# Kernel tuning notes

Measured on AMD Instinct MI355X. Metric: run time of the kernel, lower is better.

The kernel has to match this reference:

```python
import jax, jax.numpy as jnp
import numpy as np

B, CI, HI, WI = 64, 3, 96, 96
G = 8
HG, WG = 16, 16
HIDLIN = 512
SIGMA_BOOST = 2.0
EPS = 1e-7
HID = (HI // 4 // 2) * (WI // 4 // 2) * 128  # 12*12*128 = 18432


def _conv(x, w, b):
    # NCHW conv, 3x3, padding 1 (matches nn.Conv2d(kernel_size=3, padding=1))
    y = jax.lax.conv_general_dilated(x, w, (1, 1), ((1, 1), (1, 1)),
                                     dimension_numbers=('NCHW', 'OIHW', 'NCHW'))
    return y + b[None, :, None, None]


def _maxpool(x, k):
    return jax.lax.reduce_window(x, -jnp.inf, jax.lax.max,
                                 (1, 1, k, k), (1, 1, k, k), 'VALID')


def setup_inputs() -> dict:
    key = jax.random.key(0)
    ks = jax.random.split(key, 22)

    def w(k, shape, fan_in):
        return jax.random.normal(k, shape, jnp.float32) * np.float32(1.0 / np.sqrt(fan_in))

    return {
        'image': jax.random.normal(ks[0], (B, CI, HI, WI), jnp.float32),
        'noise': jax.random.normal(ks[1], (B * G, 2), jnp.float32),
        # conv block 1
        'w1a': w(ks[2], (32, CI, 3, 3), CI * 9), 'b1a': jnp.zeros((32,), jnp.float32),
        'w1b': w(ks[3], (32, 32, 3, 3), 32 * 9), 'b1b': jnp.zeros((32,), jnp.float32),
        # conv block 2
        'w2a': w(ks[4], (64, 32, 3, 3), 32 * 9), 'b2a': jnp.zeros((64,), jnp.float32),
        'w2b': w(ks[5], (64, 64, 3, 3), 64 * 9), 'b2b': jnp.zeros((64,), jnp.float32),
        # conv block 3
        'w3a': w(ks[6], (128, 64, 3, 3), 64 * 9), 'b3a': jnp.zeros((128,), jnp.float32),
        'w3b': w(ks[7], (128, 128, 3, 3), 128 * 9), 'b3b': jnp.zeros((128,), jnp.float32),
        # linear head (weights stored (in, out))
        'wl1': w(ks[8], (HID, HIDLIN), HID), 'bl1': jnp.zeros((HIDLIN,), jnp.float32),
        'wl2': w(ks[9], (HIDLIN, HIDLIN), HIDLIN), 'bl2': jnp.zeros((HIDLIN,), jnp.float32),
        'wl3': w(ks[10], (HIDLIN, G * 3), HIDLIN), 'bl3': jnp.zeros((G * 3,), jnp.float32),
    }


def reference(image, noise, w1a, b1a, w1b, b1b, w2a, b2a, w2b, b2b,
              w3a, b3a, w3b, b3b, wl1, bl1, wl2, bl2, wl3, bl3):
    # --- preprocess CNN ---
    x = jax.nn.relu(_conv(image, w1a, b1a))
    x = jax.nn.relu(_conv(x, w1b, b1b))
    x = _maxpool(x, 4)
    x = jax.nn.relu(_conv(x, w2a, b2a))
    x = jax.nn.relu(_conv(x, w2b, b2b))
    x = _maxpool(x, 2)
    x = jax.nn.relu(_conv(x, w3a, b3a))
    x = jax.nn.relu(_conv(x, w3b, b3b))
    x = x.reshape(B, -1)                      # Flatten (C,H,W order, like torch .view)
    x = jax.nn.relu(x @ wl1 + bl1)
    x = jax.nn.relu(x @ wl2 + bl2)            # Linear(HIDLIN,HIDLIN) then the extra ReLU
    prep = (x @ wl3 + bl3).reshape(B * G, 3)  # (b*g, 3)

    means = prep[:, :2]                        # (b*g, 2) raw means
    sraw = prep[:, 2]
    # sparse.transform_sigmas: softplus(s + SIGMA_BOOST) + eps, scaled per spatial dim
    sig = jax.nn.softplus(sraw + SIGMA_BOOST) + EPS
    sigmas = sig[:, None] * jnp.array([HI - 1, WI - 1], jnp.float32)  # (b*g, 2)

    # Normal(means, sigmas).sample() -> reparameterized but detached (torch .sample())
    sample = jax.lax.stop_gradient(means + sigmas * noise)
    # sparse.transform_means over size (hi-hg, wi-wg): sigmoid * (size-1), then round
    msize = jnp.array([HI - HG - 1, WI - WG - 1], jnp.float32)
    pts = jnp.round(jax.nn.sigmoid(sample) * msize).astype(jnp.int32).reshape(B, G, 2)

    # glimpse extraction: the original's b*g python slicing loop -> vmapped dynamic_slice
    src = jax.lax.stop_gradient(image)  # original slices image.data (no grad)

    def ext_one(img, p):
        return jax.lax.dynamic_slice(img, (jnp.int32(0), p[0], p[1]), (CI, HG, WG))

    result = jax.vmap(lambda img, ps: jax.vmap(lambda p: ext_one(img, p))(ps))(src, pts)
    # result: (B, G, CI, HG, WG)
    return result, means.reshape(B, G, 2), sigmas.reshape(B, G, 2)
```

## Files before the change

kernel.cpp:

```cpp
#include <hip/hip_runtime.h>
#include <math.h>

constexpr int BB  = 64;
constexpr int CIc = 3;
constexpr int HIc = 96, WIc = 96;
constexpr int Gc  = 8, HGc = 16, WGc = 16;
constexpr int HIDc = 18432;
constexpr int HIDLINc = 512;

using short8 = __attribute__((ext_vector_type(8))) short;
using s4     = __attribute__((ext_vector_type(4))) short;
using f32x16 = __attribute__((ext_vector_type(16))) float;

__device__ inline unsigned short bfr(float f) {
    unsigned int u = __float_as_uint(f);
    u = (u + 0x7FFFu + ((u >> 16) & 1u)) >> 16;
    return (unsigned short)u;
}
__device__ inline float ubf(unsigned short s) {
    return __uint_as_float(((unsigned int)s) << 16);
}
__device__ inline void tsplit(float v, unsigned short& H, unsigned short& M,
                              unsigned short& L) {
    unsigned int u = __float_as_uint(v);
    H = (unsigned short)(u >> 16);
    float r1 = v - __uint_as_float(u & 0xFFFF0000u);
    unsigned int u1 = __float_as_uint(r1);
    M = (unsigned short)(u1 >> 16);
    float r2 = r1 - __uint_as_float(u1 & 0xFFFF0000u);
    L = (unsigned short)(__float_as_uint(r2) >> 16);
}

__device__ __attribute__((aligned(16))) unsigned short g_wh[9216];
__device__ __attribute__((aligned(16))) unsigned short g_wm[9216];
__device__ __attribute__((aligned(16))) unsigned short g_wl[9216];

__device__ __attribute__((aligned(16))) unsigned short g_wph[276480];
__device__ __attribute__((aligned(16))) unsigned short g_wpm[276480];
__device__ __attribute__((aligned(16))) unsigned short g_wpl[276480];

__device__ inline void packN_one(const float* __restrict__ w, int CIN, int ofs,
                                 int idx)
{
    int chsz = 288 * CIN;
    int chunk = idx / chsz;
    int t = idx - chunk * chsz;
    int s = t >> 9;
    int rr = t & 511;
    int g = rr >> 8, oc32 = (rr >> 3) & 31, j = rr & 7;
    int nc16 = CIN / 16;
    int tap = s / nc16, c16 = s % nc16;
    int ci = c16 * 16 + g * 8 + j;
    int oc = chunk * 32 + oc32;
    float v = w[((size_t)oc * CIN + ci) * 9 + tap];
    unsigned short h = bfr(v);
    float r1 = v - ubf(h);
    unsigned short m = bfr(r1);
    g_wph[ofs + idx] = h; g_wpm[ofs + idx] = m; g_wpl[ofs + idx] = bfr(r1 - ubf(m));
}

__global__ void pack_all(const float* __restrict__ w1b, const float* __restrict__ w2a,
                         const float* __restrict__ w2b, const float* __restrict__ w3a,
                         const float* __restrict__ w3b)
{
    int idx = blockIdx.x * 256 + threadIdx.x;
    if (idx < 9216) {
        int j = idx & 7, oc = (idx >> 3) & 31, g = (idx >> 8) & 1, s = idx >> 9;
        int ci = 16 * (s & 1) + 8 * g + j;
        int tap = s >> 1;
        float v = w1b[(oc * 32 + ci) * 9 + tap];
        unsigned short h = bfr(v);
        float r1 = v - ubf(h);
        unsigned short m = bfr(r1);
        g_wh[idx] = h; g_wm[idx] = m; g_wl[idx] = bfr(r1 - ubf(m));
    } else if (idx < 27648) {
        packN_one(w2a, 32, 0, idx - 9216);
    } else if (idx < 64512) {
        packN_one(w2b, 64, 18432, idx - 27648);
    } else if (idx < 138240) {
        packN_one(w3a, 64, 55296, idx - 64512);
    } else if (idx < 285696) {
        packN_one(w3b, 128, 129024, idx - 138240);
    }
}

__device__ inline void bz_one(unsigned short* __restrict__ Xh,
                              unsigned short* __restrict__ Xm,
                              unsigned short* __restrict__ Xl,
                              int PAD, int C, int idx)
{
    int RING = 4 * PAD - 4;
    int ci = idx % C;
    int cell = (idx / C) % RING;
    int b = idx / (C * RING);
    int y, x;
    if (cell < PAD)          { y = 0;       x = cell; }
    else if (cell < 2 * PAD) { y = PAD - 1; x = cell - PAD; }
    else { int t = cell - 2 * PAD; y = 1 + (t >> 1); x = (t & 1) ? PAD - 1 : 0; }
    size_t a = ((size_t)(b * PAD + y) * PAD + x) * C + ci;
    Xh[a] = 0; Xm[a] = 0; Xl[a] = 0;
}

__global__ void border_all(unsigned short* X2h, unsigned short* X2m, unsigned short* X2l,
                           unsigned short* X3h, unsigned short* X3m, unsigned short* X3l,
                           unsigned short* X4h, unsigned short* X4m, unsigned short* X4l,
                           unsigned short* X5h, unsigned short* X5m, unsigned short* X5l)
{
    int idx = blockIdx.x * 256 + threadIdx.x;
    if (idx < 204800)        bz_one(X2h, X2m, X2l, 26, 32, idx);
    else if (idx < 614400)   bz_one(X3h, X3m, X3l, 26, 64, idx - 204800);
    else if (idx < 827392)   bz_one(X4h, X4m, X4l, 14, 64, idx - 614400);
    else if (idx < 1253376)  bz_one(X5h, X5m, X5l, 14, 128, idx - 827392);
}

__global__ __launch_bounds__(256, 5)
void conv1ab(const float* __restrict__ image, const float* __restrict__ w1a,
             const float* __restrict__ b1a, const float* __restrict__ b1b,
             unsigned short* __restrict__ X2h, unsigned short* __restrict__ X2m,
             unsigned short* __restrict__ X2l)
{
    const int id    = blockIdx.x;
    const int xcd   = id & 7;
    const int local = id >> 3;
    const int gblk  = xcd * 576 + local;
    const int b  = gblk / 72;
    const int r  = gblk % 72;
    const int yq = r / 3;
    const int xt = r % 3;

    const int tid = threadIdx.x;
    const int wave = tid >> 6, lane = tid & 63;
    const int col = lane & 31, g = lane >> 5;

    __shared__ __align__(16) short s_hml[3][6][34][20];
    __shared__ __align__(16) char  s_u[4096];
    __shared__ float s_b1b[32];
    float (*s_img)[8][36]    = (float(*)[8][36])s_u;
    float (*s_pool)[8][2][16] = (float(*)[8][2][16])s_u;
    if (tid < 32) s_b1b[tid] = b1b[tid];

    for (int idx = tid; idx < 3 * 8 * 36; idx += 256) {
        int ci = idx / 288;
        int rem = idx - ci * 288;
        int rr = rem / 36, cc = rem - rr * 36;
        int gy = 4 * yq - 2 + rr, gx = 32 * xt - 2 + cc;
        float v = 0.0f;
        if (gy >= 0 && gy < 96 && gx >= 0 && gx < 96)
            v = image[((size_t)(b * 3 + ci) * 96 + gy) * 96 + gx];
        s_img[ci][rr][cc] = v;
    }
    __syncthreads();

    const int lr = (tid < 204) ? tid / 34 : 0;
    const int lc = (tid < 204) ? tid - (tid / 34) * 34 : 0;
    const int gr = 4 * yq - 1 + lr, gc = 32 * xt - 1 + lc;
    const bool valid = (tid < 204) && (gr >= 0 && gr < 96 && gc >= 0 && gc < 96);

    f32x16 acc0 = {0,0,0,0,0,0,0,0,0,0,0,0,0,0,0,0};
    f32x16 acc1 = {0,0,0,0,0,0,0,0,0,0,0,0,0,0,0,0};

#pragma unroll
    for (int half = 0; half < 2; ++half) {
        if (half) __syncthreads();

        if (tid < 204) {
            float acc[16];
#pragma unroll
            for (int oc = 0; oc < 16; ++oc) acc[oc] = 0.0f;
            if (valid) {
#pragma unroll
                for (int ci = 0; ci < 3; ++ci) {
                    float v[3][3];
#pragma unroll
                    for (int dy = 0; dy < 3; ++dy)
#pragma unroll
                        for (int dx = 0; dx < 3; ++dx)
                            v[dy][dx] = s_img[ci][lr + dy][lc + dx];
#pragma unroll
                    for (int oc = 0; oc < 16; ++oc) {
                        const float* w9 =
                            w1a + ((size_t)(half * 16 + oc) * 3 + ci) * 9;
                        float a = acc[oc];
#pragma unroll
                        for (int dy = 0; dy < 3; ++dy)
#pragma unroll
                            for (int dx = 0; dx < 3; ++dx)
                                a = fmaf(v[dy][dx], w9[dy * 3 + dx], a);
                        acc[oc] = a;
                    }
                }
            }
#pragma unroll
            for (int q = 0; q < 4; ++q) {
                s4 H, M, L;
#pragma unroll
                for (int i = 0; i < 4; ++i) {
                    int oc = q * 4 + i;
                    float v = valid ?
                        fmaxf(acc[oc] + b1a[half * 16 + oc], 0.0f) : 0.0f;
                    unsigned short h, m, l;
                    tsplit(v, h, m, l);
                    H[i] = (short)h; M[i] = (short)m; L[i] = (short)l;
                }
                *(s4*)(&s_hml[0][lr][lc][q * 4]) = H;
                *(s4*)(&s_hml[1][lr][lc][q * 4]) = M;
                *(s4*)(&s_hml[2][lr][lc][q * 4]) = L;
            }
        }
        __syncthreads();

        __builtin_amdgcn_s_setprio(1);
#pragma unroll
        for (int tap = 0; tap < 9; ++tap) {
            const int s = tap * 2 + half;
            const int dy = tap / 3, dx = tap % 3;
            const int aidx = s * 512 + g * 256 + col * 8;

            s4 a0 = *(const s4*)(&s_hml[0][wave + dy][col + dx][g * 8]);
            s4 a1 = *(const s4*)(&s_hml[0][wave + dy][col + dx][g * 8 + 4]);
            s4 b0 = *(const s4*)(&s_hml[1][wave + dy][col + dx][g * 8]);
            s4 b1 = *(const s4*)(&s_hml[1][wave + dy][col + dx][g * 8 + 4]);
            s4 c0 = *(const s4*)(&s_hml[2][wave + dy][col + dx][g * 8]);
            s4 c1 = *(const s4*)(&s_hml[2][wave + dy][col + dx][g * 8 + 4]);

            short8 bh = __builtin_shufflevector(a0, a1, 0, 1, 2, 3, 4, 5, 6, 7);
            short8 bm = __builtin_shufflevector(b0, b1, 0, 1, 2, 3, 4, 5, 6, 7);
            short8 bl = __builtin_shufflevector(c0, c1, 0, 1, 2, 3, 4, 5, 6, 7);

            short8 ah = *(const short8*)(g_wh + aidx);
            short8 am = *(const short8*)(g_wm + aidx);
            short8 al = *(const short8*)(g_wl + aidx);

            acc0 = __builtin_amdgcn_mfma_f32_32x32x16_bf16(ah, bh, acc0, 0, 0, 0);
            acc1 = __builtin_amdgcn_mfma_f32_32x32x16_bf16(ah, bm, acc1, 0, 0, 0);
            acc0 = __builtin_amdgcn_mfma_f32_32x32x16_bf16(am, bh, acc0, 0, 0, 0);
            acc1 = __builtin_amdgcn_mfma_f32_32x32x16_bf16(am, bm, acc1, 0, 0, 0);
            acc0 = __builtin_amdgcn_mfma_f32_32x32x16_bf16(al, bh, acc0, 0, 0, 0);
            acc1 = __builtin_amdgcn_mfma_f32_32x32x16_bf16(ah, bl, acc1, 0, 0, 0);
        }
        __builtin_amdgcn_s_setprio(0);
    }
    __syncthreads();

#pragma unroll
    for (int rr = 0; rr < 16; ++rr) {
        int ocr = (rr & 3) + 8 * (rr >> 2) + 4 * g;
        float v = fmaxf(acc0[rr] + acc1[rr] + s_b1b[ocr], 0.0f);
        v = fmaxf(v, __shfl_xor(v, 1));
        v = fmaxf(v, __shfl_xor(v, 2));
        if ((col & 3) == 0) s_pool[wave][col >> 2][g][rr] = v;
    }
    __syncthreads();

    {
        int oc = tid & 31, pc = tid >> 5;
        if (pc < 8) {
            int gg = (oc >> 2) & 1;
            int rr = (oc & 3) + (((oc >> 3) & 3) << 2);
            float mv = s_pool[0][pc][gg][rr];
            mv = fmaxf(mv, s_pool[1][pc][gg][rr]);
            mv = fmaxf(mv, s_pool[2][pc][gg][rr]);
            mv = fmaxf(mv, s_pool[3][pc][gg][rr]);
            unsigned short h, m, l;
            tsplit(mv, h, m, l);
            size_t oa = ((size_t)(b * 26 + yq + 1) * 26 + xt * 8 + pc + 1) * 32 + oc;
            X2h[oa] = h; X2m[oa] = m; X2l[oa] = l;
        }
    }
}

template<int CIN, int HW, int NCHUNK, int OUTMODE>
__global__ __launch_bounds__(256)
void convN_mfma(const unsigned short* __restrict__ Xh,
                const unsigned short* __restrict__ Xm,
                const unsigned short* __restrict__ Xl,
                int wofs, const float* __restrict__ bias,
                unsigned short* __restrict__ Yh,
                unsigned short* __restrict__ Ym,
                unsigned short* __restrict__ Yl,
                float* __restrict__ Yf)
{
    constexpr int PAD = HW + 2;
    constexpr int NC16 = CIN / 16;
    constexpr int CHSZ = 288 * CIN;
    constexpr int COUT = NCHUNK * 32;

    const int tid = threadIdx.x;
    const int cpx = gridDim.x >> 3;
    const int blk = (blockIdx.x & 7) * cpx + (blockIdx.x >> 3);
    const int wid = blk * 4 + (tid >> 6);
    const int lane = tid & 63;
    const int col = lane & 31, g = lane >> 5;

    const int chunk = wid % NCHUNK;
    const int wt = wid / NCHUNK;
    const int P = wt * 32 + col;
    const int b = P / (HW * HW);
    const int rem = P - b * (HW * HW);
    const int y = rem / HW, x = rem - y * HW;

    const size_t ib = ((size_t)(b * PAD + y) * PAD + x) * CIN + g * 8;
    const int wbase = wofs + chunk * CHSZ;

    f32x16 acc0 = {0,0,0,0,0,0,0,0,0,0,0,0,0,0,0,0};
    f32x16 acc1 = {0,0,0,0,0,0,0,0,0,0,0,0,0,0,0,0};

#pragma unroll
    for (int tap = 0; tap < 9; ++tap) {
        const int dy = tap / 3, dx = tap % 3;
        for (int c16 = 0; c16 < NC16; ++c16) {
            const int s = tap * NC16 + c16;
            const int aidx = wbase + s * 512 + g * 256 + col * 8;
            const size_t xo = ib + (size_t)((dy * PAD + dx) * CIN + c16 * 16);
            short8 ah = *(const short8*)(g_wph + aidx);
            short8 am = *(const short8*)(g_wpm + aidx);
            short8 al = *(const short8*)(g_wpl + aidx);
            short8 bh = *(const short8*)(Xh + xo);
            short8 bm = *(const short8*)(Xm + xo);
            short8 bl = *(const short8*)(Xl + xo);
            acc0 = __builtin_amdgcn_mfma_f32_32x32x16_bf16(ah, bh, acc0, 0, 0, 0);
            acc1 = __builtin_amdgcn_mfma_f32_32x32x16_bf16(ah, bm, acc1, 0, 0, 0);
            acc0 = __builtin_amdgcn_mfma_f32_32x32x16_bf16(am, bh, acc0, 0, 0, 0);
            acc1 = __builtin_amdgcn_mfma_f32_32x32x16_bf16(am, bm, acc1, 0, 0, 0);
            acc0 = __builtin_amdgcn_mfma_f32_32x32x16_bf16(al, bh, acc0, 0, 0, 0);
            acc1 = __builtin_amdgcn_mfma_f32_32x32x16_bf16(ah, bl, acc1, 0, 0, 0);
        }
    }

    if constexpr (OUTMODE == 0) {
        const size_t obase =
            ((size_t)(b * PAD + y + 1) * PAD + (x + 1)) * COUT + chunk * 32;
#pragma unroll
        for (int q = 0; q < 4; ++q) {
            s4 H, M, L;
#pragma unroll
            for (int i = 0; i < 4; ++i) {
                int r = q * 4 + i;
                int ocr = i + 8 * q + 4 * g;
                float v = fmaxf(acc0[r] + acc1[r] + bias[chunk * 32 + ocr], 0.0f);
                unsigned short h, m, l;
                tsplit(v, h, m, l);
                H[i] = (short)h; M[i] = (short)m; L[i] = (short)l;
            }
            *(s4*)(Yh + obase + 8 * q + 4 * g) = H;
            *(s4*)(Ym + obase + 8 * q + 4 * g) = M;
            *(s4*)(Yl + obase + 8 * q + 4 * g) = L;
        }
    } else {
#pragma unroll
        for (int r = 0; r < 16; ++r) {
            int ocr = chunk * 32 + (r & 3) + 8 * (r >> 2) + 4 * g;
            float v = fmaxf(acc0[r] + acc1[r] + bias[ocr], 0.0f);
            Yf[((size_t)(b * COUT + ocr) * HW + y) * HW + x] = v;
        }
    }
}

__global__ __launch_bounds__(256)
void pool2_pack(const float* __restrict__ t2,
                unsigned short* __restrict__ X4h,
                unsigned short* __restrict__ X4m,
                unsigned short* __restrict__ X4l)
{
    int idx = blockIdx.x * 256 + threadIdx.x;
    constexpr int TOT = BB * 144 * 64;
    if (idx >= TOT) return;
    int oc = idx & 63;
    int p = (idx >> 6) % 144;
    int b = idx / (144 * 64);
    int y = p / 12, x = p % 12;
    const float* src = t2 + ((size_t)(b * 64 + oc) * 24 + 2 * y) * 24 + 2 * x;
    float v = fmaxf(fmaxf(src[0], src[1]), fmaxf(src[24], src[25]));
    unsigned short h, m, l;
    tsplit(v, h, m, l);
    size_t oa = ((size_t)(b * 14 + y + 1) * 14 + x + 1) * 64 + oc;
    X4h[oa] = h; X4m[oa] = m; X4l[oa] = l;
}

constexpr int KSPLIT = 64;
__global__ __launch_bounds__(256)
void lin1_partial(const float* __restrict__ x, const float* __restrict__ w,
                  float* __restrict__ partial)
{
    const int j  = threadIdx.x % 64;
    const int bg = threadIdx.x / 64;
    const int jBase = blockIdx.x * 64;
    const int k  = blockIdx.y;
    const int i0 = k * 288;

    __shared__ float s_x[32][68];

    float acc[16];
#pragma unroll
    for (int u = 0; u < 16; ++u) acc[u] = 0.0f;

    for (int ib = 0; ib < 288; ib += 32) {
        __syncthreads();
        {
            int lb = threadIdx.x / 4;
            int lo = (threadIdx.x % 4) * 8;
            const float* src = x + (size_t)lb * HIDc + i0 + ib + lo;
            float4 a0 = *(const float4*)(src);
            float4 a1 = *(const float4*)(src + 4);
            float tmp[8] = {a0.x, a0.y, a0.z, a0.w, a1.x, a1.y, a1.z, a1.w};
#pragma unroll
            for (int r = 0; r < 8; ++r) s_x[lo + r][lb] = tmp[r];
        }
        __syncthreads();

        for (int ii = 0; ii < 32; ++ii) {
            float wv = w[(size_t)(i0 + ib + ii) * HIDLINc + jBase + j];
            const float4* xp = (const float4*)&s_x[ii][bg * 16];
            float4 x0 = xp[0], x1 = xp[1], x2 = xp[2], x3 = xp[3];
            acc[0]  = fmaf(x0.x, wv, acc[0]);
            acc[1]  = fmaf(x0.y, wv, acc[1]);
            acc[2]  = fmaf(x0.z, wv, acc[2]);
            acc[3]  = fmaf(x0.w, wv, acc[3]);
            acc[4]  = fmaf(x1.x, wv, acc[4]);
            acc[5]  = fmaf(x1.y, wv, acc[5]);
            acc[6]  = fmaf(x1.z, wv, acc[6]);
            acc[7]  = fmaf(x1.w, wv, acc[7]);
            acc[8]  = fmaf(x2.x, wv, acc[8]);
            acc[9]  = fmaf(x2.y, wv, acc[9]);
            acc[10] = fmaf(x2.z, wv, acc[10]);
            acc[11] = fmaf(x2.w, wv, acc[11]);
            acc[12] = fmaf(x3.x, wv, acc[12]);
            acc[13] = fmaf(x3.y, wv, acc[13]);
            acc[14] = fmaf(x3.z, wv, acc[14]);
            acc[15] = fmaf(x3.w, wv, acc[15]);
        }
    }

#pragma unroll
    for (int u = 0; u < 16; ++u) {
        int b = bg * 16 + u;
        partial[((size_t)k * 64 + b) * HIDLINc + jBase + j] = acc[u];
    }
}

__global__ void lin1_reduce(const float* __restrict__ partial,
                            const float* __restrict__ bias,
                            float* __restrict__ x1)
{
    int idx = blockIdx.x * blockDim.x + threadIdx.x;
    if (idx >= 64 * HIDLINc) return;
    int j = idx % HIDLINc;
    float s = 0.0f;
    for (int k = 0; k < KSPLIT; ++k)
        s += partial[(size_t)k * 64 * HIDLINc + idx];
    x1[idx] = fmaxf(s + bias[j], 0.0f);
}

__global__ __launch_bounds__(256)
void lin2_k(const float* __restrict__ x1, const float* __restrict__ w,
            const float* __restrict__ bias, float* __restrict__ x2)
{
    const int j  = threadIdx.x % 64;
    const int bl = threadIdx.x / 64;
    const int jBase = blockIdx.x * 64;
    const int b = blockIdx.y * 4 + bl;

    __shared__ float s_x[4][HIDLINc];
    for (int idx = threadIdx.x; idx < 4 * HIDLINc; idx += 256)
        s_x[idx / HIDLINc][idx % HIDLINc] =
            x1[(size_t)(blockIdx.y * 4 + idx / HIDLINc) * HIDLINc + idx % HIDLINc];
    __syncthreads();

    float acc = 0.0f;
    for (int i = 0; i < HIDLINc; ++i)
        acc = fmaf(s_x[bl][i], w[(size_t)i * HIDLINc + jBase + j], acc);
    x2[(size_t)b * HIDLINc + jBase + j] = fmaxf(acc + bias[jBase + j], 0.0f);
}

__global__ void lin3_k(const float* __restrict__ x2, const float* __restrict__ w,
                       const float* __restrict__ bias, float* __restrict__ prep)
{
    int idx = blockIdx.x * blockDim.x + threadIdx.x;
    if (idx >= 64 * 24) return;
    int j = idx % 24, b = idx / 24;
    float acc = bias[j];
    for (int i = 0; i < HIDLINc; ++i)
        acc = fmaf(x2[(size_t)b * HIDLINc + i], w[i * 24 + j], acc);
    prep[idx] = acc;
}

__global__ void head_k(const float* __restrict__ prep, const float* __restrict__ noise,
                       float* __restrict__ outMeans, float* __restrict__ outSigmas,
                       int* __restrict__ pts)
{
    int id = blockIdx.x * blockDim.x + threadIdx.x;
    if (id >= BB * Gc) return;
    float m0 = prep[id * 3 + 0];
    float m1 = prep[id * 3 + 1];
    float sraw = prep[id * 3 + 2];
    float s = sraw + 2.0f;
    float sig = fmaxf(s, 0.0f) + log1pf(expf(-fabsf(s)));
    sig += 1e-7f;
    float sg = sig * 95.0f;
    outMeans[id * 2 + 0] = m0;
    outMeans[id * 2 + 1] = m1;
    outSigmas[id * 2 + 0] = sg;
    outSigmas[id * 2 + 1] = sg;
    float sa0 = m0 + sg * noise[id * 2 + 0];
    float sa1 = m1 + sg * noise[id * 2 + 1];
    float t0 = 1.0f / (1.0f + expf(-sa0));
    float t1 = 1.0f / (1.0f + expf(-sa1));
    pts[id * 2 + 0] = (int)rintf(t0 * 79.0f);
    pts[id * 2 + 1] = (int)rintf(t1 * 79.0f);
}

__global__ __launch_bounds__(256)
void patch_k(const float* __restrict__ image, const int* __restrict__ pts,
             float* __restrict__ outR)
{
    int id = blockIdx.x;
    int b = id / Gc;
    int p0 = pts[id * 2 + 0];
    int p1 = pts[id * 2 + 1];
    for (int idx = threadIdx.x; idx < CIc * HGc * WGc; idx += 256) {
        int c = idx / (HGc * WGc), rem = idx % (HGc * WGc);
        int hh = rem / WGc, ww = rem % WGc;
        outR[(size_t)id * (CIc * HGc * WGc) + idx] =
            image[((size_t)(b * CIc + c) * HIc + p0 + hh) * WIc + p1 + ww];
    }
}

extern "C" void kernel_launch(void* const* d_in, const int* in_sizes, int n_in,
                              void* d_out, int out_size, void* d_ws, size_t ws_size,
                              hipStream_t stream)
{
    const float* image = (const float*)d_in[0];
    const float* noise = (const float*)d_in[1];
    const float* w1a = (const float*)d_in[2];
    const float* b1a = (const float*)d_in[3];
    const float* w1b = (const float*)d_in[4];
    const float* b1b = (const float*)d_in[5];
    const float* w2a = (const float*)d_in[6];
    const float* b2a = (const float*)d_in[7];
    const float* w2b = (const float*)d_in[8];
    const float* b2b = (const float*)d_in[9];
    const float* w3a = (const float*)d_in[10];
    const float* b3a = (const float*)d_in[11];
    const float* w3b = (const float*)d_in[12];
    const float* b3b = (const float*)d_in[13];
    const float* wl1 = (const float*)d_in[14];
    const float* bl1 = (const float*)d_in[15];
    const float* wl2 = (const float*)d_in[16];
    const float* bl2 = (const float*)d_in[17];
    const float* wl3 = (const float*)d_in[18];
    const float* bl3 = (const float*)d_in[19];

    float* out = (float*)d_out;
    float* ws  = (float*)d_ws;

    unsigned short* X2h = (unsigned short*)(ws + 29884416);
    unsigned short* X2m = (unsigned short*)(ws + 30670848);
    unsigned short* X2l = (unsigned short*)(ws + 31457280);
    unsigned short* X3h = (unsigned short*)(ws);
    unsigned short* X3m = (unsigned short*)(ws + 1572864);
    unsigned short* X3l = (unsigned short*)(ws + 3145728);
    float*  t2  = ws + 4718592;
    unsigned short* X4h = (unsigned short*)(ws + 7340032);
    unsigned short* X4m = (unsigned short*)(ws + 7864320);
    unsigned short* X4l = (unsigned short*)(ws + 8388608);
    unsigned short* X5h = (unsigned short*)(ws + 8912896);
    unsigned short* X5m = (unsigned short*)(ws + 11010048);
    unsigned short* X5l = (unsigned short*)(ws + 12058624);
    float*  t5  = ws + 13107200;
    float*  part= ws + 14680064;
    float*  x1  = ws + 16777216;
    float*  x2  = x1 + 32768;
    float*  prep= x2 + 32768;
    int*    pts = (int*)(prep + 2048);

    pack_all<<<1116, 256, 0, stream>>>(w1b, w2a, w2b, w3a, w3b);

    border_all<<<4896, 256, 0, stream>>>(X2h, X2m, X2l, X3h, X3m, X3l,
                                         X4h, X4m, X4l, X5h, X5m, X5l);

    conv1ab<<<4608, 256, 0, stream>>>(image, w1a, b1a, b1b, X2h, X2m, X2l);

    convN_mfma<32, 24, 2, 0><<<576, 256, 0, stream>>>(
        X2h, X2m, X2l, 0, b2a, X3h, X3m, X3l, nullptr);
    convN_mfma<64, 24, 2, 1><<<576, 256, 0, stream>>>(
        X3h, X3m, X3l, 18432, b2b, nullptr, nullptr, nullptr, t2);
    pool2_pack<<<2304, 256, 0, stream>>>(t2, X4h, X4m, X4l);
    convN_mfma<64, 12, 4, 0><<<288, 256, 0, stream>>>(
        X4h, X4m, X4l, 55296, b3a, X5h, X5m, X5l, nullptr);
    convN_mfma<128, 12, 4, 1><<<288, 256, 0, stream>>>(
        X5h, X5m, X5l, 129024, b3b, nullptr, nullptr, nullptr, t5);

    lin1_partial<<<dim3(8, KSPLIT), 256, 0, stream>>>(t5, wl1, part);
    lin1_reduce<<<(64 * HIDLINc + 255) / 256, 256, 0, stream>>>(part, bl1, x1);
    lin2_k<<<dim3(8, 16), 256, 0, stream>>>(x1, wl2, bl2, x2);
    lin3_k<<<6, 256, 0, stream>>>(x2, wl3, bl3, prep);
    head_k<<<2, 256, 0, stream>>>(prep, noise,
                                  out + (size_t)BB * Gc * CIc * HGc * WGc,
                                  out + (size_t)BB * Gc * CIc * HGc * WGc + BB * Gc * 2,
                                  pts);
    patch_k<<<BB * Gc, 256, 0, stream>>>(image, pts, out);
}
```

Measured before the change: 384.9 us.

## Compute first conv layer with bf16x3 MFMA on pre-split padded image

Replaces the scalar FMA first 3x3 convolution (3->32 channels) inside conv1ab with MFMA matrix ops. A new img_split kernel pre-splits the padded image into three bf16 parts in a channel-last layout, and pack_all now packs w1a into an MFMA-friendly layout. The conv1a result is then written straight from the MFMA accumulators into shared memory for the conv1b stage. This adds an extra kernel launch, a padded image round-trip through global memory, wasted MFMA work from padding K from 27 to 48, and a lower occupancy bound.

```diff
diff --git a/kernel.cpp b/kernel.cpp
--- a/kernel.cpp
+++ b/kernel.cpp
@@ -34,6 +34,10 @@
 __device__ __attribute__((aligned(16))) unsigned short g_wh[9216];
 __device__ __attribute__((aligned(16))) unsigned short g_wm[9216];
 __device__ __attribute__((aligned(16))) unsigned short g_wl[9216];
+
+__device__ __attribute__((aligned(16))) unsigned short g_w1ah[1536];
+__device__ __attribute__((aligned(16))) unsigned short g_w1am[1536];
+__device__ __attribute__((aligned(16))) unsigned short g_w1al[1536];
 
 __device__ __attribute__((aligned(16))) unsigned short g_wph[276480];
 __device__ __attribute__((aligned(16))) unsigned short g_wpm[276480];
@@ -59,9 +63,9 @@
     g_wph[ofs + idx] = h; g_wpm[ofs + idx] = m; g_wpl[ofs + idx] = bfr(r1 - ubf(m));
 }
 
-__global__ void pack_all(const float* __restrict__ w1b, const float* __restrict__ w2a,
-                         const float* __restrict__ w2b, const float* __restrict__ w3a,
-                         const float* __restrict__ w3b)
+__global__ void pack_all(const float* __restrict__ w1a, const float* __restrict__ w1b,
+                         const float* __restrict__ w2a, const float* __restrict__ w2b,
+                         const float* __restrict__ w3a, const float* __restrict__ w3b)
 {
     int idx = blockIdx.x * 256 + threadIdx.x;
     if (idx < 9216) {
@@ -81,7 +85,43 @@
         packN_one(w3a, 64, 55296, idx - 64512);
     } else if (idx < 285696) {
         packN_one(w3b, 128, 129024, idx - 138240);
-    }
+    } else if (idx < 287232) {
+        int i2 = idx - 285696;
+        int j = i2 & 7, oc = (i2 >> 3) & 31, gg = (i2 >> 8) & 1, s = i2 >> 9;
+        int k = s * 16 + gg * 8 + j;
+        int tap = k >> 2, ci = k & 3;
+        float v = (tap < 9 && ci < 3) ? w1a[((size_t)oc * 3 + ci) * 9 + tap] : 0.0f;
+        unsigned short h = bfr(v);
+        float r1 = v - ubf(h);
+        unsigned short m = bfr(r1);
+        g_w1ah[i2] = h; g_w1am[i2] = m; g_w1al[i2] = bfr(r1 - ubf(m));
+    }
+}
+
+__global__ void img_split(const float* __restrict__ image,
+                          unsigned short* __restrict__ Ih,
+                          unsigned short* __restrict__ Im,
+                          unsigned short* __restrict__ Il)
+{
+    int idx = blockIdx.x * 256 + threadIdx.x;
+    if (idx >= 64 * 100 * 100) return;
+    int x = idx % 100;
+    int t = idx / 100;
+    int y = t % 100;
+    int b = t / 100;
+    s4 H = {0, 0, 0, 0}, M = {0, 0, 0, 0}, L = {0, 0, 0, 0};
+    if (y >= 2 && y < 98 && x >= 2 && x < 98) {
+#pragma unroll
+        for (int ci = 0; ci < 3; ++ci) {
+            float v = image[((size_t)(b * 3 + ci) * 96 + (y - 2)) * 96 + (x - 2)];
+            unsigned short hh, mm, ll;
+            tsplit(v, hh, mm, ll);
+            H[ci] = (short)hh; M[ci] = (short)mm; L[ci] = (short)ll;
+        }
+    }
+    *(s4*)(Ih + (size_t)idx * 4) = H;
+    *(s4*)(Im + (size_t)idx * 4) = M;
+    *(s4*)(Il + (size_t)idx * 4) = L;
 }
 
 __device__ inline void bz_one(unsigned short* __restrict__ Xh,
@@ -113,8 +153,10 @@
     else if (idx < 1253376)  bz_one(X5h, X5m, X5l, 14, 128, idx - 827392);
 }
 
-__global__ __launch_bounds__(256, 5)
-void conv1ab(const float* __restrict__ image, const float* __restrict__ w1a,
+__global__ __launch_bounds__(256, 4)
+void conv1ab(const unsigned short* __restrict__ Ih,
+             const unsigned short* __restrict__ Im,
+             const unsigned short* __restrict__ Il,
              const float* __restrict__ b1a, const float* __restrict__ b1b,
              unsigned short* __restrict__ X2h, unsigned short* __restrict__ X2m,
              unsigned short* __restrict__ X2l)
@@ -133,28 +175,49 @@
     const int col = lane & 31, g = lane >> 5;
 
     __shared__ __align__(16) short s_hml[3][6][34][20];
-    __shared__ __align__(16) char  s_u[4096];
-    __shared__ float s_b1b[32];
-    float (*s_img)[8][36]    = (float(*)[8][36])s_u;
-    float (*s_pool)[8][2][16] = (float(*)[8][2][16])s_u;
-    if (tid < 32) s_b1b[tid] = b1b[tid];
-
-    for (int idx = tid; idx < 3 * 8 * 36; idx += 256) {
-        int ci = idx / 288;
-        int rem = idx - ci * 288;
-        int rr = rem / 36, cc = rem - rr * 36;
-        int gy = 4 * yq - 2 + rr, gx = 32 * xt - 2 + cc;
-        float v = 0.0f;
-        if (gy >= 0 && gy < 96 && gx >= 0 && gx < 96)
-            v = image[((size_t)(b * 3 + ci) * 96 + gy) * 96 + gx];
-        s_img[ci][rr][cc] = v;
-    }
+    __shared__ float s_pool[4][8][2][16];
+    __shared__ float s_b1a[32], s_b1b[32];
+    if (tid < 32) { s_b1a[tid] = b1a[tid]; s_b1b[tid] = b1b[tid]; }
     __syncthreads();
 
-    const int lr = (tid < 204) ? tid / 34 : 0;
-    const int lc = (tid < 204) ? tid - (tid / 34) * 34 : 0;
-    const int gr = 4 * yq - 1 + lr, gc = 32 * xt - 1 + lc;
-    const bool valid = (tid < 204) && (gr >= 0 && gr < 96 && gc >= 0 && gc < 96);
+    auto convA = [&](int tile, f32x16& acc) {
+        int p = tile * 32 + col;
+        int pc = p < 204 ? p : 203;
+        int lr = pc / 34, lc = pc - (pc / 34) * 34;
+        const size_t ibase =
+            ((size_t)(b * 100 + 4 * yq + lr) * 100 + 32 * xt + lc) * 4;
+#pragma unroll
+        for (int s = 0; s < 3; ++s) {
+            int tap0 = 4 * s + 2 * g; if (tap0 > 8) tap0 = 8;
+            int tap1 = 4 * s + 2 * g + 1; if (tap1 > 8) tap1 = 8;
+            int o0 = ((tap0 / 3) * 100 + tap0 % 3) * 4;
+            int o1 = ((tap1 / 3) * 100 + tap1 % 3) * 4;
+            s4 h0 = *(const s4*)(Ih + ibase + o0);
+            s4 h1 = *(const s4*)(Ih + ibase + o1);
+            s4 m0 = *(const s4*)(Im + ibase + o0);
+            s4 m1 = *(const s4*)(Im + ibase + o1);
+            s4 l0 = *(const s4*)(Il + ibase + o0);
+            s4 l1 = *(const s4*)(Il + ibase + o1);
+            short8 bh = __builtin_shufflevector(h0, h1, 0, 1, 2, 3, 4, 5, 6, 7);
+            short8 bm = __builtin_shufflevector(m0, m1, 0, 1, 2, 3, 4, 5, 6, 7);
+            short8 bl = __builtin_shufflevector(l0, l1, 0, 1, 2, 3, 4, 5, 6, 7);
+            const int aidx = s * 512 + g * 256 + col * 8;
+            short8 ah = *(const short8*)(g_w1ah + aidx);
+            short8 am = *(const short8*)(g_w1am + aidx);
+            short8 al = *(const short8*)(g_w1al + aidx);
+            acc = __builtin_amdgcn_mfma_f32_32x32x16_bf16(ah, bh, acc, 0, 0, 0);
+            acc = __builtin_amdgcn_mfma_f32_32x32x16_bf16(ah, bm, acc, 0, 0, 0);
+            acc = __builtin_amdgcn_mfma_f32_32x32x16_bf16(am, bh, acc, 0, 0, 0);
+            acc = __builtin_amdgcn_mfma_f32_32x32x16_bf16(am, bm, acc, 0, 0, 0);
+            acc = __builtin_amdgcn_mfma_f32_32x32x16_bf16(al, bh, acc, 0, 0, 0);
+            acc = __builtin_amdgcn_mfma_f32_32x32x16_bf16(ah, bl, acc, 0, 0, 0);
+        }
+    };
+
+    f32x16 accA0 = {0,0,0,0,0,0,0,0,0,0,0,0,0,0,0,0};
+    f32x16 accA1 = {0,0,0,0,0,0,0,0,0,0,0,0,0,0,0,0};
+    convA(wave * 2, accA0);
+    if (wave != 3) convA(wave * 2 + 1, accA1);
 
     f32x16 acc0 = {0,0,0,0,0,0,0,0,0,0,0,0,0,0,0,0};
     f32x16 acc1 = {0,0,0,0,0,0,0,0,0,0,0,0,0,0,0,0};
@@ -163,48 +226,32 @@
     for (int half = 0; half < 2; ++half) {
         if (half) __syncthreads();
 
-        if (tid < 204) {
-            float acc[16];
-#pragma unroll
-            for (int oc = 0; oc < 16; ++oc) acc[oc] = 0.0f;
-            if (valid) {
-#pragma unroll
-                for (int ci = 0; ci < 3; ++ci) {
-                    float v[3][3];
-#pragma unroll
-                    for (int dy = 0; dy < 3; ++dy)
-#pragma unroll
-                        for (int dx = 0; dx < 3; ++dx)
-                            v[dy][dx] = s_img[ci][lr + dy][lc + dx];
-#pragma unroll
-                    for (int oc = 0; oc < 16; ++oc) {
-                        const float* w9 =
-                            w1a + ((size_t)(half * 16 + oc) * 3 + ci) * 9;
-                        float a = acc[oc];
-#pragma unroll
-                        for (int dy = 0; dy < 3; ++dy)
-#pragma unroll
-                            for (int dx = 0; dx < 3; ++dx)
-                                a = fmaf(v[dy][dx], w9[dy * 3 + dx], a);
-                        acc[oc] = a;
-                    }
+#pragma unroll
+        for (int t = 0; t < 2; ++t) {
+            int tile = wave * 2 + t;
+            int p = tile * 32 + col;
+            if (tile < 7 && p < 204) {
+                const f32x16& A = t ? accA1 : accA0;
+                int lr = p / 34, lc = p - (p / 34) * 34;
+                s4 H0, M0, L0, H1, M1, L1;
+#pragma unroll
+                for (int i = 0; i < 4; ++i) {
+                    float v0 = fmaxf(A[8 * half + i] +
+                                     s_b1a[16 * half + 4 * g + i], 0.0f);
+                    float v1 = fmaxf(A[8 * half + 4 + i] +
+                                     s_b1a[16 * half + 8 + 4 * g + i], 0.0f);
+                    unsigned short hh, mm, ll;
+                    tsplit(v0, hh, mm, ll);
+                    H0[i] = (short)hh; M0[i] = (short)mm; L0[i] = (short)ll;
+                    tsplit(v1, hh, mm, ll);
+                    H1[i] = (short)hh; M1[i] = (short)mm; L1[i] = (short)ll;
                 }
-            }
-#pragma unroll
-            for (int q = 0; q < 4; ++q) {
-                s4 H, M, L;
-#pragma unroll
-                for (int i = 0; i < 4; ++i) {
-                    int oc = q * 4 + i;
-                    float v = valid ?
-                        fmaxf(acc[oc] + b1a[half * 16 + oc], 0.0f) : 0.0f;
-                    unsigned short h, m, l;
-                    tsplit(v, h, m, l);
-                    H[i] = (short)h; M[i] = (short)m; L[i] = (short)l;
-                }
-                *(s4*)(&s_hml[0][lr][lc][q * 4]) = H;
-                *(s4*)(&s_hml[1][lr][lc][q * 4]) = M;
-                *(s4*)(&s_hml[2][lr][lc][q * 4]) = L;
+                *(s4*)&s_hml[0][lr][lc][4 * g]     = H0;
+                *(s4*)&s_hml[0][lr][lc][8 + 4 * g] = H1;
+                *(s4*)&s_hml[1][lr][lc][4 * g]     = M0;
+                *(s4*)&s_hml[1][lr][lc][8 + 4 * g] = M1;
+                *(s4*)&s_hml[2][lr][lc][4 * g]     = L0;
+                *(s4*)&s_hml[2][lr][lc][8 + 4 * g] = L1;
             }
         }
         __syncthreads();
@@ -572,13 +619,18 @@
     float*  x2  = x1 + 32768;
     float*  prep= x2 + 32768;
     int*    pts = (int*)(prep + 2048);
-
-    pack_all<<<1116, 256, 0, stream>>>(w1b, w2a, w2b, w3a, w3b);
+    unsigned short* Ih = (unsigned short*)(ws + 18874368);
+    unsigned short* Im = (unsigned short*)(ws + 20447232);
+    unsigned short* Il = (unsigned short*)(ws + 22020096);
+
+    pack_all<<<1122, 256, 0, stream>>>(w1a, w1b, w2a, w2b, w3a, w3b);
+
+    img_split<<<2500, 256, 0, stream>>>(image, Ih, Im, Il);
 
     border_all<<<4896, 256, 0, stream>>>(X2h, X2m, X2l, X3h, X3m, X3l,
                                          X4h, X4m, X4l, X5h, X5m, X5l);
 
-    conv1ab<<<4608, 256, 0, stream>>>(image, w1a, b1a, b1b, X2h, X2m, X2l);
+    conv1ab<<<4608, 256, 0, stream>>>(Ih, Im, Il, b1a, b1b, X2h, X2m, X2l);
 
     convN_mfma<32, 24, 2, 0><<<576, 256, 0, stream>>>(
         X2h, X2m, X2l, 0, b2a, X3h, X3m, X3l, nullptr);
```

New measurement: 358.8 us. -6.8%, faster.
